# Optimization experiments

Measured on AMD Instinct MI355X. Metric: run time of the kernel, lower is better.

## Reference

```python
import jax, jax.numpy as jnp
import numpy as np

WIN = 7
SIGMA = 1.5
C1 = 0.01 ** 2
C2 = 0.03 ** 2


def _gaussian_window(channels):
    # 1D gaussian, normalized (matches pytorch_ssim.create_window)
    xs = np.arange(WIN, dtype=np.float32)
    g = np.exp(-((xs - WIN // 2) ** 2) / (2.0 * SIGMA ** 2))
    g = g / g.sum()
    w2d = np.outer(g, g).astype(np.float32)  # [7,7], sums to 1
    # depthwise kernel [C,1,7,7] (OIHW with feature_group_count=C)
    return jnp.asarray(np.tile(w2d[None, None], (channels, 1, 1, 1)))


def _dwconv(img, win, channels):
    # img: [N,C,H,W]; 'same' padding for odd window (pad=3)
    return jax.lax.conv_general_dilated(
        img, win, window_strides=(1, 1), padding=[(3, 3), (3, 3)],
        feature_group_count=channels,
        dimension_numbers=('NCHW', 'OIHW', 'NCHW'))


def _ssim(img1, img2):
    C = img1.shape[1]
    win = _gaussian_window(C).astype(img1.dtype)
    mu1 = _dwconv(img1, win, C)
    mu2 = _dwconv(img2, win, C)
    mu1_sq = mu1 * mu1
    mu2_sq = mu2 * mu2
    mu1_mu2 = mu1 * mu2
    sigma1_sq = _dwconv(img1 * img1, win, C) - mu1_sq
    sigma2_sq = _dwconv(img2 * img2, win, C) - mu2_sq
    sigma12 = _dwconv(img1 * img2, win, C) - mu1_mu2
    ssim_map = ((2.0 * mu1_mu2 + C1) * (2.0 * sigma12 + C2)) / (
        (mu1_sq + mu2_sq + C1) * (sigma1_sq + sigma2_sq + C2))
    return jnp.mean(ssim_map)  # size_average=True


def setup_inputs() -> dict:
    key = jax.random.key(0)
    k1, k2 = jax.random.split(key)
    B, T, C, H, W = 8, 8, 3, 256, 256
    x = jax.random.uniform(k1, (B, T, C, H, W), dtype=jnp.float32)
    y = jax.random.uniform(k2, (B, T, C, H, W), dtype=jnp.float32)
    return {"x": x, "y": y}


def reference(x, y):
    # flatten(0,1): [B,T,C,H,W] -> [B*T,C,H,W]
    x2 = x.reshape((-1,) + x.shape[2:])
    y2 = y.reshape((-1,) + y.shape[2:])
    return _ssim(x2, y2)
```

## Files before the change

### kernel.cpp

```cpp
#include <hip/hip_runtime.h>

#define IMG_H 256
#define IMG_W 256
#define TW 64
#define TH 16
#define SC 72

typedef float v2f __attribute__((ext_vector_type(2)));

__device__ __forceinline__ int rotc(int r, int c) { return (c & ~7) | ((c + r) & 7); }

#define G0 0.03663285f
#define G1 0.11128076f
#define G2 0.21674532f
#define G3 0.27068216f

__global__ __launch_bounds__(256) void ssim_tile_kernel(
    const float* __restrict__ x, const float* __restrict__ y,
    float* __restrict__ partial) {
    __shared__ float4 vs[TH][SC];
    __shared__ float  wsum[4];

    const int tid = threadIdx.x;
    const int bx = blockIdx.x, by = blockIdx.y, plane = blockIdx.z;
    const int r0 = by * TH, c0 = bx * TW;
    const size_t base = (size_t)plane * (IMG_H * IMG_W);
    const float g[7] = {G0, G1, G2, G3, G2, G1, G0};

    v2f g2[7];
    #pragma unroll
    for (int d = 0; d < 7; ++d) { g2[d].x = g[d]; g2[d].y = g[d]; }

    const bool fast = ((bx == 1) | (bx == 2)) & (by >= 1) & (by <= 14);

    if (tid < 2 * SC) {
        const int a = tid / SC;
        const int c = tid - a * SC;
        const int gc = c0 - 4 + c;
        const int rstart = r0 - 3 + 8 * a;

        v2f aA[8], aB[8];
        #pragma unroll
        for (int o = 0; o < 8; ++o) { aA[o] = (v2f)0.f; aB[o] = (v2f)0.f; }

        if (fast) {
            const float* px = x + base + (size_t)rstart * IMG_W + gc;
            const float* py = y + base + (size_t)rstart * IMG_W + gc;
            #pragma unroll
            for (int t = 0; t < 14; ++t) {
                const float xv = px[t * IMG_W];
                const float yv = py[t * IMG_W];
                v2f ina; ina.x = xv; ina.y = yv;
                v2f inb; inb.x = fmaf(xv, xv, yv * yv); inb.y = xv * yv;
                #pragma unroll
                for (int o = 0; o < 8; ++o) {
                    const int dy = t - o;
                    if (dy >= 0 && dy < 7) {
                        aA[o] = __builtin_elementwise_fma(g2[dy], ina, aA[o]);
                        aB[o] = __builtin_elementwise_fma(g2[dy], inb, aB[o]);
                    }
                }
            }
        } else {
            const bool ok_c = ((unsigned)gc < IMG_W);
            const int  gcc  = gc < 0 ? 0 : (gc > IMG_W - 1 ? IMG_W - 1 : gc);
            #pragma unroll
            for (int t = 0; t < 14; ++t) {
                const int gr  = rstart + t;
                const bool ok = ok_c & ((unsigned)gr < IMG_H);
                const int grc = gr < 0 ? 0 : (gr > IMG_H - 1 ? IMG_H - 1 : gr);
                const size_t idx = base + ((size_t)grc << 8) + gcc;
                float xv = x[idx], yv = y[idx];
                xv = ok ? xv : 0.f;
                yv = ok ? yv : 0.f;
                v2f ina; ina.x = xv; ina.y = yv;
                v2f inb; inb.x = fmaf(xv, xv, yv * yv); inb.y = xv * yv;
                #pragma unroll
                for (int o = 0; o < 8; ++o) {
                    const int dy = t - o;
                    if (dy >= 0 && dy < 7) {
                        aA[o] = __builtin_elementwise_fma(g2[dy], ina, aA[o]);
                        aB[o] = __builtin_elementwise_fma(g2[dy], inb, aB[o]);
                    }
                }
            }
        }
        #pragma unroll
        for (int o = 0; o < 8; ++o) {
            const int R = 8 * a + o;
            vs[R][rotc(R, c)] = make_float4(aA[o].x, aA[o].y, aB[o].x, aB[o].y);
        }
    }

    __syncthreads();

    const int R = 4 * (tid >> 6) + (tid & 3);
    const int m = (tid >> 2) & 15;

    v2f wa[10], wb[10];
    #pragma unroll
    for (int j = 0; j < 10; ++j) {
        float4 w = vs[R][rotc(R, 4 * m + j + 1)];
        wa[j].x = w.x; wa[j].y = w.y;
        wb[j].x = w.z; wb[j].y = w.w;
    }

    const float c1 = 0.01f * 0.01f;
    const float c2 = 0.03f * 0.03f;
    float acc = 0.f;
    #pragma unroll
    for (int o = 0; o < 4; ++o) {
        v2f sab = (v2f)0.f, szw = (v2f)0.f;
        #pragma unroll
        for (int dx = 0; dx < 7; ++dx) {
            sab = __builtin_elementwise_fma(g2[dx], wa[o + dx], sab);
            szw = __builtin_elementwise_fma(g2[dx], wb[o + dx], szw);
        }
        const float sx = sab.x, sy = sab.y, szz = szw.x, sxy2 = szw.y;
        const float mu1s = sx * sx;
        const float mu2s = sy * sy;
        const float mu12 = sx * sy;
        const float s12  = sxy2 - mu12;
        const float ssum = szz - mu1s - mu2s;
        const float num  = fmaf(2.f, mu12, c1) * fmaf(2.f, s12, c2);
        const float den  = (mu1s + mu2s + c1) * (ssum + c2);
        float rcp = __builtin_amdgcn_rcpf(den);
        rcp = rcp * (2.f - den * rcp);
        acc = fmaf(num, rcp, acc);
    }

    #pragma unroll
    for (int off = 32; off > 0; off >>= 1)
        acc += __shfl_down(acc, off, 64);

    const int wave = tid >> 6;
    const int lane = tid & 63;
    if (lane == 0) wsum[wave] = acc;
    __syncthreads();
    if (tid == 0) {
        float t = wsum[0] + wsum[1] + wsum[2] + wsum[3];
        partial[((size_t)blockIdx.z * 64) + blockIdx.y * 4 + blockIdx.x] = t;
    }
}

__global__ __launch_bounds__(1024) void ssim_reduce_kernel(
    const float4* __restrict__ p, float* __restrict__ out,
    int n4, double inv_count) {
    double a = 0.0;
    for (int i = threadIdx.x; i < n4; i += 1024) {
        float4 v = p[i];
        a += (double)v.x + (double)v.y + (double)v.z + (double)v.w;
    }
    #pragma unroll
    for (int off = 32; off > 0; off >>= 1)
        a += __shfl_down(a, off, 64);
    __shared__ double sd[16];
    const int wave = threadIdx.x >> 6;
    const int lane = threadIdx.x & 63;
    if (lane == 0) sd[wave] = a;
    __syncthreads();
    if (threadIdx.x == 0) {
        double t = 0.0;
        #pragma unroll
        for (int w = 0; w < 16; w++) t += sd[w];
        out[0] = (float)(t * inv_count);
    }
}

extern "C" void kernel_launch(void* const* d_in, const int* in_sizes, int n_in,
                              void* d_out, int out_size, void* d_ws, size_t ws_size,
                              hipStream_t stream) {
    const float* x = (const float*)d_in[0];
    const float* y = (const float*)d_in[1];
    float* out = (float*)d_out;
    float* partial = (float*)d_ws;

    const int total = in_sizes[0];
    const int planes = total / (IMG_H * IMG_W);
    const int tiles_r = IMG_H / TH;
    const int tiles_c = IMG_W / TW;
    const int n_partial = planes * tiles_r * tiles_c;

    dim3 grid(tiles_c, tiles_r, planes);
    ssim_tile_kernel<<<grid, dim3(256), 0, stream>>>(x, y, partial);

    ssim_reduce_kernel<<<1, 1024, 0, stream>>>((const float4*)partial, out,
                                               n_partial / 4, 1.0 / (double)total);
}
```

Before: 49.86 us.

## Halve tile height to 8 rows with 128-thread blocks and add column-edge fast path

Shrinks each block's tile from 16 to 8 output rows and its size from 256 to 128 threads, doubling the grid. Each vertical-pass thread now produces all 8 rows, so the thread-to-tile mapping changes. A new branch handles left/right edge tiles in interior rows by multiplying loads with a column mask instead of per-row bounds checks. The aim is more blocks for occupancy and cheaper edge handling, at the cost of more redundant halo-row reads per output row (14 input rows for 8 outputs instead of 16) and twice as many partial sums.

After: 54.92 us. 10.1% more time.

```diff
diff --git a/kernel.cpp b/kernel.cpp
--- a/kernel.cpp
+++ b/kernel.cpp
@@ -3,7 +3,7 @@
 #define IMG_H 256
 #define IMG_W 256
 #define TW 64
-#define TH 16
+#define TH 8
 #define SC 72
 
 typedef float v2f __attribute__((ext_vector_type(2)));
@@ -15,11 +15,11 @@
 #define G2 0.21674532f
 #define G3 0.27068216f
 
-__global__ __launch_bounds__(256) void ssim_tile_kernel(
+__global__ __launch_bounds__(128) void ssim_tile_kernel(
     const float* __restrict__ x, const float* __restrict__ y,
     float* __restrict__ partial) {
     __shared__ float4 vs[TH][SC];
-    __shared__ float  wsum[4];
+    __shared__ float  wsum[2];
 
     const int tid = threadIdx.x;
     const int bx = blockIdx.x, by = blockIdx.y, plane = blockIdx.z;
@@ -31,25 +31,45 @@
     #pragma unroll
     for (int d = 0; d < 7; ++d) { g2[d].x = g[d]; g2[d].y = g[d]; }
 
-    const bool fast = ((bx == 1) | (bx == 2)) & (by >= 1) & (by <= 14);
-
-    if (tid < 2 * SC) {
-        const int a = tid / SC;
-        const int c = tid - a * SC;
+    const bool rows_ok = (by >= 1) & (by <= 30);
+    const bool cols_ok = (bx == 1) | (bx == 2);
+
+    if (tid < SC) {
+        const int c = tid;
         const int gc = c0 - 4 + c;
-        const int rstart = r0 - 3 + 8 * a;
+        const int rstart = r0 - 3;
 
         v2f aA[8], aB[8];
         #pragma unroll
         for (int o = 0; o < 8; ++o) { aA[o] = (v2f)0.f; aB[o] = (v2f)0.f; }
 
-        if (fast) {
+        if (rows_ok & cols_ok) {
             const float* px = x + base + (size_t)rstart * IMG_W + gc;
             const float* py = y + base + (size_t)rstart * IMG_W + gc;
             #pragma unroll
             for (int t = 0; t < 14; ++t) {
                 const float xv = px[t * IMG_W];
                 const float yv = py[t * IMG_W];
+                v2f ina; ina.x = xv; ina.y = yv;
+                v2f inb; inb.x = fmaf(xv, xv, yv * yv); inb.y = xv * yv;
+                #pragma unroll
+                for (int o = 0; o < 8; ++o) {
+                    const int dy = t - o;
+                    if (dy >= 0 && dy < 7) {
+                        aA[o] = __builtin_elementwise_fma(g2[dy], ina, aA[o]);
+                        aB[o] = __builtin_elementwise_fma(g2[dy], inb, aB[o]);
+                    }
+                }
+            }
+        } else if (rows_ok) {
+            const int  gcc = gc < 0 ? 0 : (gc > IMG_W - 1 ? IMG_W - 1 : gc);
+            const float mc = ((unsigned)gc < IMG_W) ? 1.f : 0.f;
+            const float* px = x + base + (size_t)rstart * IMG_W + gcc;
+            const float* py = y + base + (size_t)rstart * IMG_W + gcc;
+            #pragma unroll
+            for (int t = 0; t < 14; ++t) {
+                const float xv = px[t * IMG_W] * mc;
+                const float yv = py[t * IMG_W] * mc;
                 v2f ina; ina.x = xv; ina.y = yv;
                 v2f inb; inb.x = fmaf(xv, xv, yv * yv); inb.y = xv * yv;
                 #pragma unroll
@@ -87,15 +107,14 @@
         }
         #pragma unroll
         for (int o = 0; o < 8; ++o) {
-            const int R = 8 * a + o;
-            vs[R][rotc(R, c)] = make_float4(aA[o].x, aA[o].y, aB[o].x, aB[o].y);
+            vs[o][rotc(o, c)] = make_float4(aA[o].x, aA[o].y, aB[o].x, aB[o].y);
         }
     }
 
     __syncthreads();
 
-    const int R = 4 * (tid >> 6) + (tid & 3);
-    const int m = (tid >> 2) & 15;
+    const int R = tid & 7;
+    const int m = tid >> 3;
 
     v2f wa[10], wb[10];
     #pragma unroll
@@ -138,8 +157,7 @@
     if (lane == 0) wsum[wave] = acc;
     __syncthreads();
     if (tid == 0) {
-        float t = wsum[0] + wsum[1] + wsum[2] + wsum[3];
-        partial[((size_t)blockIdx.z * 64) + blockIdx.y * 4 + blockIdx.x] = t;
+        partial[((size_t)plane * 128) + by * 4 + bx] = wsum[0] + wsum[1];
     }
 }
 
@@ -182,7 +200,7 @@
     const int n_partial = planes * tiles_r * tiles_c;
 
     dim3 grid(tiles_c, tiles_r, planes);
-    ssim_tile_kernel<<<grid, dim3(256), 0, stream>>>(x, y, partial);
+    ssim_tile_kernel<<<grid, dim3(128), 0, stream>>>(x, y, partial);
 
     ssim_reduce_kernel<<<1, 1024, 0, stream>>>((const float4*)partial, out,
                                                n_partial / 4, 1.0 / (double)total);
```
